# Kernel tuning notes

Measured on AMD Instinct MI355X. Metric: run time of the kernel, lower is better.

## Reference

```python
import jax, jax.numpy as jnp
import numpy as np

N_NODES = 100000
N_EDGES = 1600000
N_FEAT = 64
HIDDEN = 64
N_GRAPHS = 64
N_CLASSES = 2


def setup_inputs() -> dict:
    key = jax.random.key(0)
    ks = jax.random.split(key, 12)
    x = jax.random.normal(ks[0], (N_NODES, N_FEAT), dtype=jnp.float32)
    edge_index = jax.random.randint(ks[1], (2, N_EDGES), 0, N_NODES, dtype=jnp.int32)
    batch = jnp.sort(jax.random.randint(ks[2], (N_NODES,), 0, N_GRAPHS, dtype=jnp.int32))
    # Glorot-style init for GCNConv weights, zeros for biases (PyG default)
    def glorot(k, fan_in, fan_out):
        s = jnp.sqrt(6.0 / (fan_in + fan_out))
        return jax.random.uniform(k, (fan_in, fan_out), jnp.float32, -s, s)
    W1 = glorot(ks[3], N_FEAT, HIDDEN); b1 = jnp.zeros((HIDDEN,), jnp.float32)
    W2 = glorot(ks[4], HIDDEN, HIDDEN); b2 = jnp.zeros((HIDDEN,), jnp.float32)
    W3 = glorot(ks[5], HIDDEN, HIDDEN); b3 = jnp.zeros((HIDDEN,), jnp.float32)
    Wl = glorot(ks[6], HIDDEN, N_CLASSES); bl = jnp.zeros((N_CLASSES,), jnp.float32)
    return {"x": x, "edge_index": edge_index, "batch": batch,
            "W1": W1, "b1": b1, "W2": W2, "b2": b2, "W3": W3, "b3": b3,
            "Wl": Wl, "bl": bl}


def _gcn_conv(h, W, b, src, dst, dinv, n_nodes):
    # GCNConv with self-loops: out_i = sum_j d_i^-1/2 d_j^-1/2 (x_j W) + d_i^-1 (x_i W) + b
    h = h @ W                                   # [N, H]
    coef = (dinv[src] * dinv[dst])[:, None]     # [E, 1]
    agg = jax.ops.segment_sum(coef * h[src], dst, num_segments=n_nodes)
    return agg + (dinv * dinv)[:, None] * h + b


def reference(x, edge_index, batch, W1, b1, W2, b2, W3, b3, Wl, bl):
    src, dst = edge_index[0], edge_index[1]
    # degree of A + I (edge weight 1), shared by all three convs
    deg = jax.ops.segment_sum(jnp.ones((N_EDGES,), x.dtype), dst, num_segments=N_NODES) + 1.0
    dinv = jax.lax.rsqrt(deg)

    h = jax.nn.relu(_gcn_conv(x, W1, b1, src, dst, dinv, N_NODES))
    h = jax.nn.relu(_gcn_conv(h, W2, b2, src, dst, dinv, N_NODES))
    h = _gcn_conv(h, W3, b3, src, dst, dinv, N_NODES)

    # global_mean_pool over graph ids
    sums = jax.ops.segment_sum(h, batch, num_segments=N_GRAPHS)
    cnts = jax.ops.segment_sum(jnp.ones((N_NODES,), x.dtype), batch, num_segments=N_GRAPHS)
    pooled = sums / jnp.maximum(cnts, 1.0)[:, None]

    # dropout(p=0.5) is identity in eval mode
    return pooled @ Wl + bl
```

## Files before the change

kernel.cpp:

```cpp
#include <hip/hip_runtime.h>


#define NF 64
#define ELLW 64
#define BINSHIFT 9
#define BINW 512
#define NB 196
#define BINCAP 9216
#define LPITCH 68

typedef __attribute__((ext_vector_type(8))) _Float16 f16x8;
typedef __attribute__((ext_vector_type(4))) _Float16 f16x4;
typedef __attribute__((ext_vector_type(4))) float f32x4;

__device__ inline unsigned short f2h_u(float f) {
    return __builtin_bit_cast(unsigned short, (_Float16)f);
}
__device__ inline unsigned int pack_h2(float a, float b) {
    unsigned int ua = f2h_u(a), ub = f2h_u(b);
    return ua | (ub << 16);
}

__global__ void binA_kernel(const int* __restrict__ src, const int* __restrict__ dst,
                            int* __restrict__ binCnt, int* __restrict__ binEdges,
                            int nE, int chunk) {
    __shared__ int hist[NB];
    __shared__ int base[NB];
    int t = threadIdx.x;
    if (t < NB) hist[t] = 0;
    __syncthreads();
    int e0 = blockIdx.x * chunk;
    int e1 = min(e0 + chunk, nE);
    for (int e = e0 + t; e < e1; e += blockDim.x) {
        int b = dst[e] >> BINSHIFT;
        atomicAdd(&hist[b], 1);
    }
    __syncthreads();
    if (t < NB) {
        base[t] = atomicAdd(&binCnt[t], hist[t]);
        hist[t] = 0;
    }
    __syncthreads();
    for (int e = e0 + t; e < e1; e += blockDim.x) {
        int d = dst[e];
        int b = d >> BINSHIFT;
        int pos = base[b] + atomicAdd(&hist[b], 1);
        if (pos < BINCAP)
            binEdges[(size_t)b * BINCAP + pos] = src[e] | ((d & (BINW - 1)) << 17);
    }
}

__global__ void __launch_bounds__(512) binB_kernel(const int* __restrict__ binEdges,
                            const int* __restrict__ binCnt, int* __restrict__ cnt,
                            float* __restrict__ dinv, int* __restrict__ colELL, int n,
                            unsigned int* __restrict__ dummyA, unsigned int* __restrict__ dummyB) {
    __shared__ int lcnt[BINW];
    int t = threadIdx.x;
    int b = blockIdx.x;
    if (b == 0 && t < 32) { dummyA[t] = 0u; dummyB[t] = 0u; }
    for (int i = t; i < BINW; i += blockDim.x) lcnt[i] = 1;
    __syncthreads();
    int m = binCnt[b];
    if (m > BINCAP) m = BINCAP;
    const int* be = binEdges + (size_t)b * BINCAP;
    int nbase = b << BINSHIFT;
    for (int e = t; e < m; e += blockDim.x) {
        int v = be[e];
        int s = v & 0x1FFFF;
        int dl = v >> 17;
        int pos = atomicAdd(&lcnt[dl], 1);
        if (pos < ELLW) colELL[(size_t)(nbase + dl) * ELLW + pos] = s;
    }
    __syncthreads();
    for (int i = t; i < BINW; i += blockDim.x) {
        int node = nbase + i;
        if (node < n) {
            int c = lcnt[i];
            if (c > ELLW) c = ELLW;
            colELL[(size_t)node * ELLW + 0] = node;
            int cpad = (c + 3) & ~3;
            for (int j = c; j < cpad; ++j)
                colELL[(size_t)node * ELLW + j] = n;
            cnt[node] = c;
            dinv[node] = rsqrtf((float)c);
        }
    }
}

__global__ void prep_kernel(const float* __restrict__ W1, const float* __restrict__ W2,
                            const float* __restrict__ W3, unsigned short* __restrict__ w1h,
                            unsigned short* __restrict__ w2h, unsigned short* __restrict__ w3h) {
    int t = blockIdx.x * blockDim.x + threadIdx.x;
    if (t < NF * NF) {
        w1h[t] = f2h_u(W1[t]);
        w2h[t] = f2h_u(W2[t]);
        w3h[t] = f2h_u(W3[t]);
    }
}

__device__ inline void load_W_frags(const unsigned short* __restrict__ Wh, int r16, int kq,
                                    f16x8 bfr[4][2]) {
#pragma unroll
    for (int nt = 0; nt < 4; ++nt)
#pragma unroll
        for (int kh = 0; kh < 2; ++kh) {
            f16x8 f;
#pragma unroll
            for (int j = 0; j < 8; ++j)
                f[j] = __builtin_bit_cast(_Float16,
                        Wh[(kh * 32 + kq * 8 + j) * NF + nt * 16 + r16]);
            bfr[nt][kh] = f;
        }
}

__global__ void __launch_bounds__(256) gemm1_mfma_kernel(const float* __restrict__ A,
                                                         const unsigned short* __restrict__ Wh,
                                                         const float* __restrict__ dinv,
                                                         unsigned short* __restrict__ outB, int n) {
    __shared__ unsigned short T[4][16 * LPITCH];
    int lane = threadIdx.x & 63;
    int r16 = lane & 15, kq = lane >> 4;
    int wv = threadIdx.x >> 6;
    int wid = blockIdx.x * 4 + wv;
    int nw = gridDim.x * 4;
    f16x8 bfr[4][2];
    load_W_frags(Wh, r16, kq, bfr);
    int ntiles = n >> 4;
    for (int t = wid; t < ntiles; t += nw) {
        int r0 = t << 4;
        const float* ar = A + (size_t)(r0 + r16) * NF + kq * 8;
        f16x8 a0, a1;
        float4 v0 = *(const float4*)(ar);
        float4 v1 = *(const float4*)(ar + 4);
        float4 v2 = *(const float4*)(ar + 32);
        float4 v3 = *(const float4*)(ar + 36);
        a0[0] = (_Float16)v0.x; a0[1] = (_Float16)v0.y;
        a0[2] = (_Float16)v0.z; a0[3] = (_Float16)v0.w;
        a0[4] = (_Float16)v1.x; a0[5] = (_Float16)v1.y;
        a0[6] = (_Float16)v1.z; a0[7] = (_Float16)v1.w;
        a1[0] = (_Float16)v2.x; a1[1] = (_Float16)v2.y;
        a1[2] = (_Float16)v2.z; a1[3] = (_Float16)v2.w;
        a1[4] = (_Float16)v3.x; a1[5] = (_Float16)v3.y;
        a1[6] = (_Float16)v3.z; a1[7] = (_Float16)v3.w;
        f32x4 acc[4];
#pragma unroll
        for (int nt = 0; nt < 4; ++nt) {
            acc[nt] = (f32x4)(0.0f);
            acc[nt] = __builtin_amdgcn_mfma_f32_16x16x32_f16(a0, bfr[nt][0], acc[nt], 0, 0, 0);
            acc[nt] = __builtin_amdgcn_mfma_f32_16x16x32_f16(a1, bfr[nt][1], acc[nt], 0, 0, 0);
        }
        float ds[4];
#pragma unroll
        for (int reg = 0; reg < 4; ++reg) ds[reg] = dinv[r0 + kq * 4 + reg];
        unsigned short* Tw = T[wv];
#pragma unroll
        for (int nt = 0; nt < 4; ++nt)
#pragma unroll
            for (int reg = 0; reg < 4; ++reg)
                Tw[(kq * 4 + reg) * LPITCH + nt * 16 + r16] = f2h_u(acc[nt][reg] * ds[reg]);
#pragma unroll
        for (int it = 0; it < 4; ++it) {
            int row = it * 4 + kq;
            uint2 v = *(const uint2*)&Tw[row * LPITCH + r16 * 4];
            *(uint2*)(outB + (size_t)(r0 + row) * NF + r16 * 4) = v;
        }
    }
}

__global__ void __launch_bounds__(256) fused_agg_gemm_kernel(
        const unsigned short* __restrict__ hB, const int* __restrict__ colELL,
        const int* __restrict__ cnt, const float* __restrict__ dinv,
        const float* __restrict__ bias, const unsigned short* __restrict__ Wh,
        unsigned short* __restrict__ outB, int n) {
    __shared__ int Icol[16 * 32];
    __shared__ int Icnt[16];
    __shared__ unsigned short Tin[2048];
    __shared__ unsigned short Tout[16 * LPITCH];
    int lane = threadIdx.x & 63;
    int wv = threadIdx.x >> 6;
    int es = lane >> 4, fq = lane & 15;
    int r16 = lane & 15, kq = lane >> 4;
    int r0 = blockIdx.x << 4;
    if (threadIdx.x < 128) {
        int srow = threadIdx.x >> 3, sj = threadIdx.x & 7;
        ((int4*)Icol)[srow * 8 + sj] =
            *(const int4*)(colELL + (size_t)(r0 + srow) * ELLW + sj * 4);
    } else if (threadIdx.x < 144) {
        Icnt[threadIdx.x - 128] = cnt[r0 + threadIdx.x - 128];
    }
    f16x8 bfr0, bfr1;
    {
        f16x8 f0, f1;
#pragma unroll
        for (int j = 0; j < 8; ++j) {
            f0[j] = __builtin_bit_cast(_Float16, Wh[(kq * 8 + j) * NF + wv * 16 + r16]);
            f1[j] = __builtin_bit_cast(_Float16, Wh[(32 + kq * 8 + j) * NF + wv * 16 + r16]);
        }
        bfr0 = f0; bfr1 = f1;
    }
    __syncthreads();
#pragma unroll
    for (int rr = 0; rr < 4; ++rr) {
        int lrow = wv * 4 + rr;
        int row = r0 + lrow;
        int c = Icnt[lrow];
        int nq = (c + 3) >> 2;
        int nqL = nq < 8 ? nq : 8;
        const int* cr = Icol + lrow * 32;
        float a0 = 0.f, a1 = 0.f, a2 = 0.f, a3 = 0.f;
        int q = 0;
        for (; q + 4 <= nqL; q += 4) {
            int s0 = cr[q * 4 + es];
            int s1 = cr[q * 4 + 4 + es];
            int s2 = cr[q * 4 + 8 + es];
            int s3 = cr[q * 4 + 12 + es];
            f16x4 h0 = __builtin_bit_cast(f16x4, *(const uint2*)(hB + (size_t)s0 * NF + fq * 4));
            f16x4 h1 = __builtin_bit_cast(f16x4, *(const uint2*)(hB + (size_t)s1 * NF + fq * 4));
            f16x4 h2 = __builtin_bit_cast(f16x4, *(const uint2*)(hB + (size_t)s2 * NF + fq * 4));
            f16x4 h3 = __builtin_bit_cast(f16x4, *(const uint2*)(hB + (size_t)s3 * NF + fq * 4));
            f16x4 tt = (h0 + h1) + (h2 + h3);
            a0 += (float)tt[0]; a1 += (float)tt[1];
            a2 += (float)tt[2]; a3 += (float)tt[3];
        }
        for (; q + 2 <= nqL; q += 2) {
            int s0 = cr[q * 4 + es];
            int s1 = cr[q * 4 + 4 + es];
            f16x4 h0 = __builtin_bit_cast(f16x4, *(const uint2*)(hB + (size_t)s0 * NF + fq * 4));
            f16x4 h1 = __builtin_bit_cast(f16x4, *(const uint2*)(hB + (size_t)s1 * NF + fq * 4));
            f16x4 tt = h0 + h1;
            a0 += (float)tt[0]; a1 += (float)tt[1];
            a2 += (float)tt[2]; a3 += (float)tt[3];
        }
        if (q < nqL) {
            int s0 = cr[q * 4 + es];
            f16x4 h0 = __builtin_bit_cast(f16x4, *(const uint2*)(hB + (size_t)s0 * NF + fq * 4));
            a0 += (float)h0[0]; a1 += (float)h0[1];
            a2 += (float)h0[2]; a3 += (float)h0[3];
        }
        if (nq > 8) {
            const int* crg = colELL + (size_t)row * ELLW;
            for (int qq = 8; qq < nq; ++qq) {
                int s0 = crg[qq * 4 + es];
                f16x4 h0 = __builtin_bit_cast(f16x4, *(const uint2*)(hB + (size_t)s0 * NF + fq * 4));
                a0 += (float)h0[0]; a1 += (float)h0[1];
                a2 += (float)h0[2]; a3 += (float)h0[3];
            }
        }
        a0 += __shfl_xor(a0, 16); a1 += __shfl_xor(a1, 16);
        a2 += __shfl_xor(a2, 16); a3 += __shfl_xor(a3, 16);
        a0 += __shfl_xor(a0, 32); a1 += __shfl_xor(a1, 32);
        a2 += __shfl_xor(a2, 32); a3 += __shfl_xor(a3, 32);
        if (es == 0) {
            float dd = dinv[row];
            float4 b4 = *(const float4*)(bias + fq * 4);
            a0 = fmaxf(dd * a0 + b4.x, 0.f); a1 = fmaxf(dd * a1 + b4.y, 0.f);
            a2 = fmaxf(dd * a2 + b4.z, 0.f); a3 = fmaxf(dd * a3 + b4.w, 0.f);
            uint2 v;
            v.x = pack_h2(a0, a1);
            v.y = pack_h2(a2, a3);
            int ibase = ((fq >> 3) << 10) + (((fq >> 1) & 3) << 7)
                      + (wv * 4 + rr) * 8 + ((fq & 1) << 2);
            *(uint2*)&Tin[ibase] = v;
        }
    }
    __syncthreads();
    f16x8 A0 = *(const f16x8*)&Tin[lane * 8];
    f16x8 A1 = *(const f16x8*)&Tin[1024 + lane * 8];
    f32x4 acc = (f32x4)(0.0f);
    acc = __builtin_amdgcn_mfma_f32_16x16x32_f16(A0, bfr0, acc, 0, 0, 0);
    acc = __builtin_amdgcn_mfma_f32_16x16x32_f16(A1, bfr1, acc, 0, 0, 0);
    float ds[4];
#pragma unroll
    for (int reg = 0; reg < 4; ++reg) ds[reg] = dinv[r0 + kq * 4 + reg];
#pragma unroll
    for (int reg = 0; reg < 4; ++reg)
        Tout[(kq * 4 + reg) * LPITCH + wv * 16 + r16] = f2h_u(acc[reg] * ds[reg]);
    __syncthreads();
    int t = threadIdx.x;
    int orow = t >> 4, ocq = t & 15;
    uint2 v = *(const uint2*)&Tout[orow * LPITCH + ocq * 4];
    *(uint2*)(outB + (size_t)(r0 + orow) * NF + ocq * 4) = v;
}

__global__ void __launch_bounds__(256) gather3_pool_kernel(
        const unsigned short* __restrict__ hB, const int* __restrict__ colELL,
        const int* __restrict__ cnt, const float* __restrict__ dinv,
        const float* __restrict__ bias, const int* __restrict__ batch,
        float* __restrict__ pooled, int n) {
    __shared__ int Icol[32 * 32];
    __shared__ int Icnt[32];
    __shared__ int Ibatch[32];
    __shared__ float PL[2][NF];
    int t = threadIdx.x;
    int lane = t & 63;
    int wv = t >> 6;
    int es = lane >> 3;
    int fq = lane & 7;
    int r0 = blockIdx.x << 5;
    {
        int srow = t >> 3, sj = t & 7;
        ((int4*)Icol)[t] = *(const int4*)(colELL + (size_t)(r0 + srow) * ELLW + sj * 4);
    }
    if (t < 32) { Icnt[t] = cnt[r0 + t]; Ibatch[t] = batch[r0 + t]; }
    if (t >= 128) PL[(t - 128) >> 6][t & 63] = 0.f;
    __syncthreads();
    int lrow = wv * 8 + es;
    int row = r0 + lrow;
    int c = Icnt[lrow];
    int cpad = (c + 3) & ~3;
    int cl4 = cpad < 32 ? cpad : 32;
    const int* cr = Icol + lrow * 32;
    float acc[8];
#pragma unroll
    for (int j = 0; j < 8; ++j) acc[j] = 0.f;
    for (int q = 0; q + 4 <= cl4; q += 4) {
        int s0 = cr[q], s1 = cr[q + 1], s2 = cr[q + 2], s3 = cr[q + 3];
        f16x8 h0 = *(const f16x8*)(hB + (size_t)s0 * NF + fq * 8);
        f16x8 h1 = *(const f16x8*)(hB + (size_t)s1 * NF + fq * 8);
        f16x8 h2 = *(const f16x8*)(hB + (size_t)s2 * NF + fq * 8);
        f16x8 h3 = *(const f16x8*)(hB + (size_t)s3 * NF + fq * 8);
        f16x8 tt = (h0 + h1) + (h2 + h3);
#pragma unroll
        for (int j = 0; j < 8; ++j) acc[j] += (float)tt[j];
    }
    if (c > 32) {
        const int* crg = colELL + (size_t)row * ELLW;
        for (int qq = 32; qq + 4 <= cpad; qq += 4) {
            int s0 = crg[qq], s1 = crg[qq + 1], s2 = crg[qq + 2], s3 = crg[qq + 3];
            f16x8 h0 = *(const f16x8*)(hB + (size_t)s0 * NF + fq * 8);
            f16x8 h1 = *(const f16x8*)(hB + (size_t)s1 * NF + fq * 8);
            f16x8 h2 = *(const f16x8*)(hB + (size_t)s2 * NF + fq * 8);
            f16x8 h3 = *(const f16x8*)(hB + (size_t)s3 * NF + fq * 8);
            f16x8 tt = (h0 + h1) + (h2 + h3);
#pragma unroll
            for (int j = 0; j < 8; ++j) acc[j] += (float)tt[j];
        }
    }
    float dd = dinv[row];
    float4 bA = *(const float4*)(bias + fq * 8);
    float4 bB = *(const float4*)(bias + fq * 8 + 4);
    float r[8];
    r[0] = dd * acc[0] + bA.x; r[1] = dd * acc[1] + bA.y;
    r[2] = dd * acc[2] + bA.z; r[3] = dd * acc[3] + bA.w;
    r[4] = dd * acc[4] + bB.x; r[5] = dd * acc[5] + bB.y;
    r[6] = dd * acc[6] + bB.z; r[7] = dd * acc[7] + bB.w;
    int g = Ibatch[lrow];
    int gb = Ibatch[0];
    int sel = g - gb;
    if (sel < 2) {
#pragma unroll
        for (int j = 0; j < 8; ++j) atomicAdd(&PL[sel][fq * 8 + j], r[j]);
    } else {
#pragma unroll
        for (int j = 0; j < 8; ++j) atomicAdd(&pooled[g * NF + fq * 8 + j], r[j]);
    }
    __syncthreads();
    if (t < 128) {
        int s = t >> 6, f = t & 63;
        float v = PL[s][f];
        if (v != 0.f) atomicAdd(&pooled[(gb + s) * NF + f], v);
    }
}

__global__ void counts_kernel(const int* __restrict__ batch, float* __restrict__ counts, int n) {
    __shared__ int h[64];
    int t = threadIdx.x;
    if (t < 64) h[t] = 0;
    __syncthreads();
    for (int i = blockIdx.x * blockDim.x + t; i < n; i += gridDim.x * blockDim.x)
        atomicAdd(&h[batch[i]], 1);
    __syncthreads();
    if (t < 64 && h[t] > 0) atomicAdd(&counts[t], (float)h[t]);
}

__global__ void final_kernel(const float* __restrict__ pooled, const float* __restrict__ counts,
                             const float* __restrict__ Wl, const float* __restrict__ bl,
                             float* __restrict__ out) {
    int t = threadIdx.x;
    int g = t >> 1, c = t & 1;
    float inv = 1.0f / fmaxf(counts[g], 1.0f);
    float s = 0.0f;
#pragma unroll
    for (int j = 0; j < NF; ++j) s += pooled[g * NF + j] * Wl[j * 2 + c];
    out[t] = s * inv + bl[c];
}

extern "C" void kernel_launch(void* const* d_in, const int* in_sizes, int n_in,
                              void* d_out, int out_size, void* d_ws, size_t ws_size,
                              hipStream_t stream) {
    const float* x     = (const float*)d_in[0];
    const int*   ei    = (const int*)d_in[1];
    const int*   batch = (const int*)d_in[2];
    const float* W1    = (const float*)d_in[3];
    const float* b1    = (const float*)d_in[4];
    const float* W2    = (const float*)d_in[5];
    const float* b2    = (const float*)d_in[6];
    const float* W3    = (const float*)d_in[7];
    const float* b3    = (const float*)d_in[8];
    const float* Wl    = (const float*)d_in[9];
    const float* bl    = (const float*)d_in[10];
    float* out = (float*)d_out;

    const int n  = in_sizes[0] / NF;
    const int nE = in_sizes[1] / 2;
    const int* src = ei;
    const int* dst = ei + nE;

    char* ws = (char*)d_ws;
    auto alloc = [&](size_t bytes) {
        char* p = ws;
        ws += (bytes + 255) & ~(size_t)255;
        return p;
    };
    unsigned short* bufA = (unsigned short*)alloc((size_t)(n + 16) * NF * 2);
    unsigned short* bufB = (unsigned short*)alloc((size_t)(n + 16) * NF * 2);
    float* scratch = (float*)alloc((size_t)n * NF * 4);
    int*   binEdges = (int*)scratch;
    int*   colELL = (int*)alloc((size_t)n * ELLW * 4);
    float* dinv   = (float*)alloc((size_t)(n + 16) * 4);
    int*   cnt    = (int*)alloc((size_t)n * 4);
    unsigned short* w1h = (unsigned short*)alloc((size_t)NF * NF * 2);
    unsigned short* w2h = (unsigned short*)alloc((size_t)NF * NF * 2);
    unsigned short* w3h = (unsigned short*)alloc((size_t)NF * NF * 2);
    char*  ztail  = ws;
    int*   binCnt = (int*)alloc(NB * 4);
    float* pooled = (float*)alloc(64 * NF * 4);
    float* counts = (float*)alloc(64 * 4);
    size_t zbytes = (size_t)(ws - ztail);

    (void)hipMemsetAsync(ztail, 0, zbytes, stream);

    const int chunk = 3200;
    binA_kernel<<<(nE + chunk - 1) / chunk, 256, 0, stream>>>(src, dst, binCnt, binEdges, nE, chunk);
    binB_kernel<<<NB, 512, 0, stream>>>(binEdges, binCnt, cnt, dinv, colELL, n,
                                        (unsigned int*)(bufA + (size_t)n * NF),
                                        (unsigned int*)(bufB + (size_t)n * NF));
    counts_kernel<<<98, 1024, 0, stream>>>(batch, counts, n);
    prep_kernel<<<16, 256, 0, stream>>>(W1, W2, W3, w1h, w2h, w3h);

    const int tile_grid = n >> 4;

    gemm1_mfma_kernel<<<1563, 256, 0, stream>>>(x, w1h, dinv, bufA, n);
    fused_agg_gemm_kernel<<<tile_grid, 256, 0, stream>>>(bufA, colELL, cnt, dinv, b1, w2h, bufB, n);
    fused_agg_gemm_kernel<<<tile_grid, 256, 0, stream>>>(bufB, colELL, cnt, dinv, b2, w3h, bufA, n);
    gather3_pool_kernel<<<n >> 5, 256, 0, stream>>>(bufA, colELL, cnt, dinv, b3,
                                                    batch, pooled, n);

    final_kernel<<<1, 128, 0, stream>>>(pooled, counts, Wl, bl, out);
}
```

Baseline: 255.9 us.

## Restructure fused aggregate-GEMM to 32-row tiles with 8-wide per-lane gathers

The fused aggregation+GEMM kernel now handles 32 rows per block instead of 16. Each group of 8 lanes owns a whole row and gathers 16-byte f16x8 vectors per neighbour, where before 4 edge-lanes each did 8-byte loads. This removes the cross-lane shuffle reduction and raises the bytes per gather load. The MFMA stage now has each wave compute two 16-column slices of one of two 16-row tiles, and output stores use 16-byte writes. The cost is more registers for the B fragments and fewer blocks in the grid, so per-row work may be less balanced.

```diff
diff --git a/kernel.cpp b/kernel.cpp
--- a/kernel.cpp
+++ b/kernel.cpp
@@ -172,114 +172,111 @@
         const int* __restrict__ cnt, const float* __restrict__ dinv,
         const float* __restrict__ bias, const unsigned short* __restrict__ Wh,
         unsigned short* __restrict__ outB, int n) {
-    __shared__ int Icol[16 * 32];
-    __shared__ int Icnt[16];
-    __shared__ unsigned short Tin[2048];
-    __shared__ unsigned short Tout[16 * LPITCH];
-    int lane = threadIdx.x & 63;
-    int wv = threadIdx.x >> 6;
-    int es = lane >> 4, fq = lane & 15;
+    __shared__ int Icol[32 * 32];
+    __shared__ int Icnt[32];
+    __shared__ unsigned short Tin[2][2048];
+    __shared__ unsigned short Tout[2][16 * LPITCH];
+    int t = threadIdx.x;
+    int lane = t & 63;
+    int wv = t >> 6;
+    int es = lane >> 3;
+    int fq = lane & 7;
     int r16 = lane & 15, kq = lane >> 4;
-    int r0 = blockIdx.x << 4;
-    if (threadIdx.x < 128) {
-        int srow = threadIdx.x >> 3, sj = threadIdx.x & 7;
-        ((int4*)Icol)[srow * 8 + sj] =
-            *(const int4*)(colELL + (size_t)(r0 + srow) * ELLW + sj * 4);
-    } else if (threadIdx.x < 144) {
-        Icnt[threadIdx.x - 128] = cnt[r0 + threadIdx.x - 128];
-    }
-    f16x8 bfr0, bfr1;
+    int r0 = (int)(blockIdx.x << 5);
     {
-        f16x8 f0, f1;
-#pragma unroll
-        for (int j = 0; j < 8; ++j) {
-            f0[j] = __builtin_bit_cast(_Float16, Wh[(kq * 8 + j) * NF + wv * 16 + r16]);
-            f1[j] = __builtin_bit_cast(_Float16, Wh[(32 + kq * 8 + j) * NF + wv * 16 + r16]);
-        }
-        bfr0 = f0; bfr1 = f1;
-    }
-    __syncthreads();
-#pragma unroll
-    for (int rr = 0; rr < 4; ++rr) {
-        int lrow = wv * 4 + rr;
-        int row = r0 + lrow;
-        int c = Icnt[lrow];
-        int nq = (c + 3) >> 2;
-        int nqL = nq < 8 ? nq : 8;
-        const int* cr = Icol + lrow * 32;
-        float a0 = 0.f, a1 = 0.f, a2 = 0.f, a3 = 0.f;
-        int q = 0;
-        for (; q + 4 <= nqL; q += 4) {
-            int s0 = cr[q * 4 + es];
-            int s1 = cr[q * 4 + 4 + es];
-            int s2 = cr[q * 4 + 8 + es];
-            int s3 = cr[q * 4 + 12 + es];
-            f16x4 h0 = __builtin_bit_cast(f16x4, *(const uint2*)(hB + (size_t)s0 * NF + fq * 4));
-            f16x4 h1 = __builtin_bit_cast(f16x4, *(const uint2*)(hB + (size_t)s1 * NF + fq * 4));
-            f16x4 h2 = __builtin_bit_cast(f16x4, *(const uint2*)(hB + (size_t)s2 * NF + fq * 4));
-            f16x4 h3 = __builtin_bit_cast(f16x4, *(const uint2*)(hB + (size_t)s3 * NF + fq * 4));
-            f16x4 tt = (h0 + h1) + (h2 + h3);
-            a0 += (float)tt[0]; a1 += (float)tt[1];
-            a2 += (float)tt[2]; a3 += (float)tt[3];
-        }
-        for (; q + 2 <= nqL; q += 2) {
-            int s0 = cr[q * 4 + es];
-            int s1 = cr[q * 4 + 4 + es];
-            f16x4 h0 = __builtin_bit_cast(f16x4, *(const uint2*)(hB + (size_t)s0 * NF + fq * 4));
-            f16x4 h1 = __builtin_bit_cast(f16x4, *(const uint2*)(hB + (size_t)s1 * NF + fq * 4));
-            f16x4 tt = h0 + h1;
-            a0 += (float)tt[0]; a1 += (float)tt[1];
-            a2 += (float)tt[2]; a3 += (float)tt[3];
-        }
-        if (q < nqL) {
-            int s0 = cr[q * 4 + es];
-            f16x4 h0 = __builtin_bit_cast(f16x4, *(const uint2*)(hB + (size_t)s0 * NF + fq * 4));
-            a0 += (float)h0[0]; a1 += (float)h0[1];
-            a2 += (float)h0[2]; a3 += (float)h0[3];
-        }
-        if (nq > 8) {
-            const int* crg = colELL + (size_t)row * ELLW;
-            for (int qq = 8; qq < nq; ++qq) {
-                int s0 = crg[qq * 4 + es];
-                f16x4 h0 = __builtin_bit_cast(f16x4, *(const uint2*)(hB + (size_t)s0 * NF + fq * 4));
-                a0 += (float)h0[0]; a1 += (float)h0[1];
-                a2 += (float)h0[2]; a3 += (float)h0[3];
-            }
-        }
-        a0 += __shfl_xor(a0, 16); a1 += __shfl_xor(a1, 16);
-        a2 += __shfl_xor(a2, 16); a3 += __shfl_xor(a3, 16);
-        a0 += __shfl_xor(a0, 32); a1 += __shfl_xor(a1, 32);
-        a2 += __shfl_xor(a2, 32); a3 += __shfl_xor(a3, 32);
-        if (es == 0) {
-            float dd = dinv[row];
-            float4 b4 = *(const float4*)(bias + fq * 4);
-            a0 = fmaxf(dd * a0 + b4.x, 0.f); a1 = fmaxf(dd * a1 + b4.y, 0.f);
-            a2 = fmaxf(dd * a2 + b4.z, 0.f); a3 = fmaxf(dd * a3 + b4.w, 0.f);
-            uint2 v;
-            v.x = pack_h2(a0, a1);
-            v.y = pack_h2(a2, a3);
-            int ibase = ((fq >> 3) << 10) + (((fq >> 1) & 3) << 7)
-                      + (wv * 4 + rr) * 8 + ((fq & 1) << 2);
-            *(uint2*)&Tin[ibase] = v;
-        }
-    }
-    __syncthreads();
-    f16x8 A0 = *(const f16x8*)&Tin[lane * 8];
-    f16x8 A1 = *(const f16x8*)&Tin[1024 + lane * 8];
-    f32x4 acc = (f32x4)(0.0f);
-    acc = __builtin_amdgcn_mfma_f32_16x16x32_f16(A0, bfr0, acc, 0, 0, 0);
-    acc = __builtin_amdgcn_mfma_f32_16x16x32_f16(A1, bfr1, acc, 0, 0, 0);
+        int srow = t >> 3, sj = t & 7;
+        ((int4*)Icol)[t] = *(const int4*)(colELL + (size_t)(r0 + srow) * ELLW + sj * 4);
+    }
+    if (t < 32) Icnt[t] = cnt[r0 + t];
+    int s0 = (wv & 1) << 1;
+    f16x8 bfr[2][2];
+#pragma unroll
+    for (int si = 0; si < 2; ++si)
+#pragma unroll
+        for (int kh = 0; kh < 2; ++kh) {
+            f16x8 f;
+#pragma unroll
+            for (int j = 0; j < 8; ++j)
+                f[j] = __builtin_bit_cast(_Float16,
+                        Wh[(kh * 32 + kq * 8 + j) * NF + (s0 + si) * 16 + r16]);
+            bfr[si][kh] = f;
+        }
+    __syncthreads();
+    int lrow = wv * 8 + es;
+    int row = r0 + lrow;
+    int c = Icnt[lrow];
+    int cpad = (c + 3) & ~3;
+    int cl4 = cpad < 32 ? cpad : 32;
+    const int* cr = Icol + lrow * 32;
+    float acc[8];
+#pragma unroll
+    for (int j = 0; j < 8; ++j) acc[j] = 0.f;
+    for (int q = 0; q + 4 <= cl4; q += 4) {
+        int s0e = cr[q], s1e = cr[q + 1], s2e = cr[q + 2], s3e = cr[q + 3];
+        f16x8 h0 = *(const f16x8*)(hB + (size_t)s0e * NF + fq * 8);
+        f16x8 h1 = *(const f16x8*)(hB + (size_t)s1e * NF + fq * 8);
+        f16x8 h2 = *(const f16x8*)(hB + (size_t)s2e * NF + fq * 8);
+        f16x8 h3 = *(const f16x8*)(hB + (size_t)s3e * NF + fq * 8);
+        f16x8 tt = (h0 + h1) + (h2 + h3);
+#pragma unroll
+        for (int j = 0; j < 8; ++j) acc[j] += (float)tt[j];
+    }
+    if (c > 32) {
+        const int* crg = colELL + (size_t)row * ELLW;
+        for (int qq = 32; qq + 4 <= cpad; qq += 4) {
+            int s0e = crg[qq], s1e = crg[qq + 1], s2e = crg[qq + 2], s3e = crg[qq + 3];
+            f16x8 h0 = *(const f16x8*)(hB + (size_t)s0e * NF + fq * 8);
+            f16x8 h1 = *(const f16x8*)(hB + (size_t)s1e * NF + fq * 8);
+            f16x8 h2 = *(const f16x8*)(hB + (size_t)s2e * NF + fq * 8);
+            f16x8 h3 = *(const f16x8*)(hB + (size_t)s3e * NF + fq * 8);
+            f16x8 tt = (h0 + h1) + (h2 + h3);
+#pragma unroll
+            for (int j = 0; j < 8; ++j) acc[j] += (float)tt[j];
+        }
+    }
+    {
+        float dd = dinv[row];
+        float4 bA = *(const float4*)(bias + fq * 8);
+        float4 bB = *(const float4*)(bias + fq * 8 + 4);
+        float r0f = fmaxf(dd * acc[0] + bA.x, 0.f), r1f = fmaxf(dd * acc[1] + bA.y, 0.f);
+        float r2f = fmaxf(dd * acc[2] + bA.z, 0.f), r3f = fmaxf(dd * acc[3] + bA.w, 0.f);
+        float r4f = fmaxf(dd * acc[4] + bB.x, 0.f), r5f = fmaxf(dd * acc[5] + bB.y, 0.f);
+        float r6f = fmaxf(dd * acc[6] + bB.z, 0.f), r7f = fmaxf(dd * acc[7] + bB.w, 0.f);
+        int4 v;
+        v.x = (int)pack_h2(r0f, r1f);
+        v.y = (int)pack_h2(r2f, r3f);
+        v.z = (int)pack_h2(r4f, r5f);
+        v.w = (int)pack_h2(r6f, r7f);
+        int tile = lrow >> 4;
+        int idx = ((fq >> 2) << 10) + (((fq & 3) * 16 + (lrow & 15)) << 3);
+        *(int4*)&Tin[tile][idx] = v;
+    }
+    __syncthreads();
+    int tile = wv >> 1;
+    f16x8 A0 = *(const f16x8*)&Tin[tile][lane * 8];
+    f16x8 A1 = *(const f16x8*)&Tin[tile][1024 + lane * 8];
     float ds[4];
 #pragma unroll
-    for (int reg = 0; reg < 4; ++reg) ds[reg] = dinv[r0 + kq * 4 + reg];
-#pragma unroll
-    for (int reg = 0; reg < 4; ++reg)
-        Tout[(kq * 4 + reg) * LPITCH + wv * 16 + r16] = f2h_u(acc[reg] * ds[reg]);
-    __syncthreads();
-    int t = threadIdx.x;
-    int orow = t >> 4, ocq = t & 15;
-    uint2 v = *(const uint2*)&Tout[orow * LPITCH + ocq * 4];
-    *(uint2*)(outB + (size_t)(r0 + orow) * NF + ocq * 4) = v;
+    for (int reg = 0; reg < 4; ++reg) ds[reg] = dinv[r0 + tile * 16 + kq * 4 + reg];
+#pragma unroll
+    for (int si = 0; si < 2; ++si) {
+        f32x4 accC = (f32x4)(0.0f);
+        accC = __builtin_amdgcn_mfma_f32_16x16x32_f16(A0, bfr[si][0], accC, 0, 0, 0);
+        accC = __builtin_amdgcn_mfma_f32_16x16x32_f16(A1, bfr[si][1], accC, 0, 0, 0);
+#pragma unroll
+        for (int reg = 0; reg < 4; ++reg)
+            Tout[tile][(kq * 4 + reg) * LPITCH + (s0 + si) * 16 + r16] =
+                f2h_u(accC[reg] * ds[reg]);
+    }
+    __syncthreads();
+    {
+        int orow = t >> 3, oc = t & 7;
+        const unsigned short* p = &Tout[orow >> 4][(orow & 15) * LPITCH + oc * 8];
+        uint2 v0 = *(const uint2*)(p);
+        uint2 v1 = *(const uint2*)(p + 4);
+        int4 v; v.x = (int)v0.x; v.y = (int)v0.y; v.z = (int)v1.x; v.w = (int)v1.y;
+        *(int4*)(outB + (size_t)(r0 + orow) * NF + oc * 8) = v;
+    }
 }
 
 __global__ void __launch_bounds__(256) gather3_pool_kernel(
@@ -296,7 +293,7 @@
     int wv = t >> 6;
     int es = lane >> 3;
     int fq = lane & 7;
-    int r0 = blockIdx.x << 5;
+    int r0 = (int)(blockIdx.x << 5);
     {
         int srow = t >> 3, sj = t & 7;
         ((int4*)Icol)[t] = *(const int4*)(colELL + (size_t)(r0 + srow) * ELLW + sj * 4);
@@ -438,11 +435,9 @@
     counts_kernel<<<98, 1024, 0, stream>>>(batch, counts, n);
     prep_kernel<<<16, 256, 0, stream>>>(W1, W2, W3, w1h, w2h, w3h);
 
-    const int tile_grid = n >> 4;
-
     gemm1_mfma_kernel<<<1563, 256, 0, stream>>>(x, w1h, dinv, bufA, n);
-    fused_agg_gemm_kernel<<<tile_grid, 256, 0, stream>>>(bufA, colELL, cnt, dinv, b1, w2h, bufB, n);
-    fused_agg_gemm_kernel<<<tile_grid, 256, 0, stream>>>(bufB, colELL, cnt, dinv, b2, w3h, bufA, n);
+    fused_agg_gemm_kernel<<<n >> 5, 256, 0, stream>>>(bufA, colELL, cnt, dinv, b1, w2h, bufB, n);
+    fused_agg_gemm_kernel<<<n >> 5, 256, 0, stream>>>(bufB, colELL, cnt, dinv, b2, w3h, bufA, n);
     gather3_pool_kernel<<<n >> 5, 256, 0, stream>>>(bufA, colELL, cnt, dinv, b3,
                                                     batch, pooled, n);
 
```

Result: no change. 252.2 us (-1.4%).
